# Optimization experiments

Hardware: AMD Instinct MI355X
Metric: run time of the kernel (lower is better)

Reference implementation:

```python
import jax, jax.numpy as jnp
import numpy as np

N_UNARY = 16
N_BINARY = 4
N_NODES = 100000
N_EDGES = 1600000
N_CLAUSES = 8

# Parsed unary clauses: clause i = nU{i}, U{i+1}, U{i+2}
U_IDX = np.array([[i, i + 1, i + 2] for i in range(N_CLAUSES)], dtype=np.int32)
U_SGN = np.tile(np.array([[-1.0, 1.0, 1.0]], dtype=np.float32), (N_CLAUSES, 1))
# Parsed binary clauses over joined matrix [Ux(0:16), Uy(16:32), B(32:36)]:
# clause i = nU{i}x, B{i%4}, U{i}y
B_IDX = np.array([[i, 32 + (i % 4), 16 + i] for i in range(N_CLAUSES)], dtype=np.int32)
B_SGN = np.tile(np.array([[-1.0, 1.0, 1.0]], dtype=np.float32), (N_CLAUSES, 1))


def knowledge_enhancer(x, idx, sgn, w):
    """KENN clause deltas: gather literal columns, softmax(signs*x), scatter-add.
    x: [n, width], idx/sgn: [n_clauses, 3], w: [n_clauses] -> delta [n, width]."""
    sel = x[:, idx] * sgn  # [n, n_clauses, 3]
    d = (w[:, None] * sgn) * jax.nn.softmax(sel, axis=-1)  # [n, n_clauses, 3]
    return jnp.zeros_like(x).at[:, idx].add(d)


def setup_inputs() -> dict:
    key = jax.random.key(0)
    k1, k2, k3, k4 = jax.random.split(key, 4)
    unary = jax.random.normal(k1, (N_NODES, N_UNARY), dtype=jnp.float32)
    binary = jax.random.normal(k2, (N_EDGES, N_BINARY), dtype=jnp.float32)
    index1 = jax.random.randint(k3, (N_EDGES,), 0, N_NODES)
    index2 = jax.random.randint(k4, (N_EDGES,), 0, N_NODES)
    unary_cw = jnp.full((N_CLAUSES,), 0.5, dtype=jnp.float32)
    binary_cw = jnp.full((N_CLAUSES,), 0.5, dtype=jnp.float32)
    return {"unary": unary, "binary": binary, "unary_cw": unary_cw,
            "binary_cw": binary_cw, "index1": index1, "index2": index2}


def reference(unary, binary, unary_cw, binary_cw, index1, index2):
    # Unary knowledge enhancement
    u = unary + knowledge_enhancer(unary, U_IDX, U_SGN, unary_cw)
    # Join: gather endpoint unary features, concat with binary preactivations
    joined = jnp.concatenate([u[index1], u[index2], binary], axis=1)  # [E, 36]
    db = knowledge_enhancer(joined, B_IDX, B_SGN, binary_cw)  # [E, 36]
    # GroupBy: scatter unary parts back to nodes, keep binary part on edges
    delta_up = (jnp.zeros_like(u)
                .at[index1].add(db[:, :N_UNARY])
                .at[index2].add(db[:, N_UNARY:2 * N_UNARY]))
    delta_bp = db[:, 2 * N_UNARY:]
    # activation is identity (default lambda x: x)
    return u + delta_up, binary + delta_bp
```

## Files before the change

### kernel.cpp

```cpp
#include <hip/hip_runtime.h>
#include <math.h>


#define NU 16
#define NC 8
#define TILE_N 400u
#define NB 512
#define BT 512
#define CACHE_N 3200
#define ACC_ST 400
#define BTA 1024

typedef float    f32x4 __attribute__((ext_vector_type(4)));
typedef unsigned u32x4 __attribute__((ext_vector_type(4)));

__device__ __forceinline__ int q10(float x) {
    int q = __float2int_rn(x * 512.0f);
    q = q < -511 ? -511 : (q > 511 ? 511 : q);
    return q & 0x3FF;
}
__device__ __forceinline__ int sx10(unsigned w, int sh) {
    return ((int)(w << (22 - sh))) >> 22;
}
__device__ __forceinline__ unsigned long long pk4(int a0, int a1, int a2, int a3) {
    return (unsigned long long)(long long)a0 +
           ((unsigned long long)(long long)a1 << 16) +
           ((unsigned long long)(long long)a2 << 32) +
           ((unsigned long long)(unsigned short)a3 << 48);
}

__global__ void unary_enhance_kernel(const float* __restrict__ unary,
                                     const float* __restrict__ ucw,
                                     float* __restrict__ out_u,
                                     float* __restrict__ u_lo,
                                     unsigned* __restrict__ cursor,
                                     int n_nodes, int T) {
    int n = blockIdx.x * blockDim.x + threadIdx.x;
    if (cursor && n < T) cursor[n] = 0u;
    if (n >= n_nodes) return;

    float x[NU];
    const float4* src = (const float4*)(unary + (size_t)n * NU);
#pragma unroll
    for (int j = 0; j < 4; ++j) {
        float4 v = src[j];
        x[4*j+0] = v.x; x[4*j+1] = v.y; x[4*j+2] = v.z; x[4*j+3] = v.w;
    }
    float dlt[NU];
#pragma unroll
    for (int j = 0; j < NU; ++j) dlt[j] = 0.0f;
#pragma unroll
    for (int i = 0; i < NC; ++i) {
        float w = ucw[i];
        float a = -x[i], b = x[i+1], c = x[i+2];
        float m = fmaxf(a, fmaxf(b, c));
        float e0 = __expf(a - m);
        float e1 = __expf(b - m);
        float e2 = __expf(c - m);
        float inv = 1.0f / (e0 + e1 + e2);
        dlt[i]   -= w * e0 * inv;
        dlt[i+1] += w * e1 * inv;
        dlt[i+2] += w * e2 * inv;
    }
    float u[NU];
#pragma unroll
    for (int j = 0; j < NU; ++j) u[j] = x[j] + dlt[j];

    float4* dst = (float4*)(out_u + (size_t)n * NU);
#pragma unroll
    for (int j = 0; j < 4; ++j) {
        float4 v; v.x = u[4*j+0]; v.y = u[4*j+1]; v.z = u[4*j+2]; v.w = u[4*j+3];
        dst[j] = v;
    }
    float4* lo = (float4*)(u_lo + (size_t)n * 8);
    float4 l0; l0.x = u[0]; l0.y = u[1]; l0.z = u[2]; l0.w = u[3];
    float4 l1; l1.x = u[4]; l1.y = u[5]; l1.z = u[6]; l1.w = u[7];
    lo[0] = l0; lo[1] = l1;
}

__device__ __forceinline__ void edge_body(int e, int i1, int i2, f32x4 bv,
                                          float4 a0, float4 a1, float4 c0, float4 c1,
                                          const float* w,
                                          float* __restrict__ out_b,
                                          unsigned* hist,
                                          unsigned* __restrict__ entries,
                                          float* __restrict__ out_u,
                                          int cap) {
    float b[4] = {bv.x, bv.y, bv.z, bv.w};
    float u1[8] = {a0.x,a0.y,a0.z,a0.w,a1.x,a1.y,a1.z,a1.w};
    float u2[8] = {c0.x,c0.y,c0.z,c0.w,c1.x,c1.y,c1.z,c1.w};

    float d1[8], d2[8], dbp[4] = {0.f,0.f,0.f,0.f};
#pragma unroll
    for (int i = 0; i < NC; ++i) {
        float a = -u1[i], bb = b[i & 3], c = u2[i];
        float m = fmaxf(a, fmaxf(bb, c));
        float e0x = __expf(a - m);
        float e1x = __expf(bb - m);
        float e2x = __expf(c - m);
        float inv = 1.0f / (e0x + e1x + e2x);
        d1[i] = -w[i] * e0x * inv;
        d2[i] =  w[i] * e2x * inv;
        dbp[i & 3] += w[i] * e1x * inv;
    }
    f32x4 ob;
    ob.x = b[0] + dbp[0];
    ob.y = b[1] + dbp[1];
    ob.z = b[2] + dbp[2];
    ob.w = b[3] + dbp[3];
    __builtin_nontemporal_store(ob, ((f32x4*)out_b) + e);

    unsigned t1 = (unsigned)i1 / TILE_N;
    unsigned id1 = (unsigned)i1 - t1 * TILE_N;
    unsigned slot1 = atomicAdd(&hist[t1], 1u);
    if (slot1 < (unsigned)cap) {
        unsigned* ep = entries + ((size_t)t1 * cap + slot1) * 3;
        ep[0] = (unsigned)q10(d1[0]) | ((unsigned)q10(d1[1]) << 10) | ((unsigned)q10(d1[2]) << 20);
        ep[1] = (unsigned)q10(d1[3]) | ((unsigned)q10(d1[4]) << 10) | ((unsigned)q10(d1[5]) << 20);
        ep[2] = (unsigned)q10(d1[6]) | ((unsigned)q10(d1[7]) << 10) | (id1 << 20);
    } else {
        float* r = out_u + (size_t)i1 * NU;
#pragma unroll
        for (int i = 0; i < NC; ++i) atomicAdd(r + i, d1[i]);
    }

    unsigned t2 = (unsigned)i2 / TILE_N;
    unsigned id2 = (unsigned)i2 - t2 * TILE_N;
    unsigned slot2 = atomicAdd(&hist[t2], 1u);
    if (slot2 < (unsigned)cap) {
        unsigned* ep = entries + ((size_t)t2 * cap + slot2) * 3;
        ep[0] = (unsigned)q10(d2[0]) | ((unsigned)q10(d2[1]) << 10) | ((unsigned)q10(d2[2]) << 20);
        ep[1] = (unsigned)q10(d2[3]) | ((unsigned)q10(d2[4]) << 10) | ((unsigned)q10(d2[5]) << 20);
        ep[2] = (unsigned)q10(d2[6]) | ((unsigned)q10(d2[7]) << 10) | (id2 << 20);
    } else {
        float* r = out_u + (size_t)i2 * NU;
#pragma unroll
        for (int i = 0; i < NC; ++i) atomicAdd(r + i, d2[i]);
    }
}

__global__ __launch_bounds__(BT, 4)
void bin_edges_kernel(const float* __restrict__ binary,
                      const float* __restrict__ bcw,
                      const int* __restrict__ index1,
                      const int* __restrict__ index2,
                      const float* __restrict__ u_lo,
                      float* __restrict__ out_b,
                      unsigned* __restrict__ cursor,
                      unsigned* __restrict__ entries,
                      float* __restrict__ out_u,
                      int n_edges, int T, int cap, int chunk) {
    __shared__ unsigned hist[256];
    __shared__ int ic1[CACHE_N];
    __shared__ int ic2[CACHE_N];
    int tid = threadIdx.x;
    for (int t = tid; t < T; t += BT) hist[t] = 0u;
    __syncthreads();

    int e0 = blockIdx.x * chunk;
    int e1 = e0 + chunk; if (e1 > n_edges) e1 = n_edges;

    for (int e = e0 + tid; e < e1; e += BT) {
        int i1 = __builtin_nontemporal_load(index1 + e);
        int i2 = __builtin_nontemporal_load(index2 + e);
        int l = e - e0;
        ic1[l] = i1;
        ic2[l] = i2;
        atomicAdd(&hist[(unsigned)i1 / TILE_N], 1u);
        atomicAdd(&hist[(unsigned)i2 / TILE_N], 1u);
    }
    __syncthreads();

    for (int t = tid; t < T; t += BT) {
        unsigned c = hist[t];
        unsigned base = 0u;
        if (c) base = atomicAdd(&cursor[t], c);
        hist[t] = base;
    }
    __syncthreads();

    float w[NC];
#pragma unroll
    for (int i = 0; i < NC; ++i) w[i] = bcw[i];

    int eA = e0 + tid;
    for (; eA + 3 * BT < e1; eA += 4 * BT) {
        int eB = eA + BT, eC = eA + 2 * BT, eD = eA + 3 * BT;
        int lA = eA - e0, lB = eB - e0, lC = eC - e0, lD = eD - e0;
        int i1A = ic1[lA], i2A = ic2[lA];
        int i1B = ic1[lB], i2B = ic2[lB];
        int i1C = ic1[lC], i2C = ic2[lC];
        int i1D = ic1[lD], i2D = ic2[lD];

        f32x4 bvA = __builtin_nontemporal_load(((const f32x4*)binary) + eA);
        f32x4 bvB = __builtin_nontemporal_load(((const f32x4*)binary) + eB);
        f32x4 bvC = __builtin_nontemporal_load(((const f32x4*)binary) + eC);
        f32x4 bvD = __builtin_nontemporal_load(((const f32x4*)binary) + eD);

        const float4* p1A = (const float4*)(u_lo + (size_t)i1A * 8);
        const float4* p2A = (const float4*)(u_lo + (size_t)i2A * 8);
        const float4* p1B = (const float4*)(u_lo + (size_t)i1B * 8);
        const float4* p2B = (const float4*)(u_lo + (size_t)i2B * 8);
        const float4* p1C = (const float4*)(u_lo + (size_t)i1C * 8);
        const float4* p2C = (const float4*)(u_lo + (size_t)i2C * 8);
        const float4* p1D = (const float4*)(u_lo + (size_t)i1D * 8);
        const float4* p2D = (const float4*)(u_lo + (size_t)i2D * 8);
        float4 a0A = p1A[0], a1A = p1A[1], c0A = p2A[0], c1A = p2A[1];
        float4 a0B = p1B[0], a1B = p1B[1], c0B = p2B[0], c1B = p2B[1];
        float4 a0C = p1C[0], a1C = p1C[1], c0C = p2C[0], c1C = p2C[1];
        float4 a0D = p1D[0], a1D = p1D[1], c0D = p2D[0], c1D = p2D[1];

        edge_body(eA, i1A, i2A, bvA, a0A, a1A, c0A, c1A,
                  w, out_b, hist, entries, out_u, cap);
        edge_body(eB, i1B, i2B, bvB, a0B, a1B, c0B, c1B,
                  w, out_b, hist, entries, out_u, cap);
        edge_body(eC, i1C, i2C, bvC, a0C, a1C, c0C, c1C,
                  w, out_b, hist, entries, out_u, cap);
        edge_body(eD, i1D, i2D, bvD, a0D, a1D, c0D, c1D,
                  w, out_b, hist, entries, out_u, cap);
    }
    for (; eA < e1; eA += BT) {
        int lA = eA - e0;
        int i1A = ic1[lA], i2A = ic2[lA];
        f32x4 bvA = __builtin_nontemporal_load(((const f32x4*)binary) + eA);
        const float4* p1A = (const float4*)(u_lo + (size_t)i1A * 8);
        const float4* p2A = (const float4*)(u_lo + (size_t)i2A * 8);
        float4 a0A = p1A[0], a1A = p1A[1];
        float4 c0A = p2A[0], c1A = p2A[1];
        edge_body(eA, i1A, i2A, bvA, a0A, a1A, c0A, c1A,
                  w, out_b, hist, entries, out_u, cap);
    }
}

__global__ __launch_bounds__(BTA)
void tile_acc_kernel(const unsigned* __restrict__ cursor,
                     const unsigned* __restrict__ entries,
                     float* __restrict__ out_u,
                     int n_nodes, int cap) {
    __shared__ unsigned long long acc[2 * ACC_ST];
    int t = blockIdx.x;
    int tid = threadIdx.x;
    for (int i = tid; i < 2 * ACC_ST; i += BTA) acc[i] = 0ull;
    __syncthreads();

    unsigned cnt = cursor[t];
    if (cnt > (unsigned)cap) cnt = (unsigned)cap;
    size_t base = (size_t)t * cap;

    unsigned cnt4 = cnt & ~3u;
    for (unsigned i = (unsigned)tid * 4; i < cnt4; i += BTA * 4) {
        const u32x4* p = (const u32x4*)(entries + (base + i) * 3);
        u32x4 q0 = __builtin_nontemporal_load(p + 0);
        u32x4 q1 = __builtin_nontemporal_load(p + 1);
        u32x4 q2 = __builtin_nontemporal_load(p + 2);
        unsigned d[12] = {q0.x, q0.y, q0.z, q0.w,
                          q1.x, q1.y, q1.z, q1.w,
                          q2.x, q2.y, q2.z, q2.w};
#pragma unroll
        for (int k = 0; k < 4; ++k) {
            unsigned wx = d[3*k], wy = d[3*k+1], wz = d[3*k+2];
            unsigned id = wz >> 20;
            unsigned long long lo = pk4(sx10(wx, 0), sx10(wx, 10), sx10(wx, 20), sx10(wy, 0));
            unsigned long long hi = pk4(sx10(wy, 10), sx10(wy, 20), sx10(wz, 0), sx10(wz, 10));
            atomicAdd(&acc[id], lo);
            atomicAdd(&acc[ACC_ST + id], hi);
        }
    }
    for (unsigned i = cnt4 + tid; i < cnt; i += BTA) {
        const unsigned* ep = entries + (base + i) * 3;
        unsigned wx = ep[0], wy = ep[1], wz = ep[2];
        unsigned id = wz >> 20;
        unsigned long long lo = pk4(sx10(wx, 0), sx10(wx, 10), sx10(wx, 20), sx10(wy, 0));
        unsigned long long hi = pk4(sx10(wy, 10), sx10(wy, 20), sx10(wz, 0), sx10(wz, 10));
        atomicAdd(&acc[id], lo);
        atomicAdd(&acc[ACC_ST + id], hi);
    }
    __syncthreads();

    const float INV = 1.0f / 512.0f;
    int nbase = t * (int)TILE_N;
    for (int l = tid; l < (int)TILE_N; l += BTA) {
        int n = nbase + l;
        if (n >= n_nodes) continue;
        float col[8];
#pragma unroll
        for (int wd = 0; wd < 2; ++wd) {
            unsigned long long S = acc[wd*ACC_ST + l];
#pragma unroll
            for (int f = 0; f < 4; ++f) {
                short s = (short)(S & 0xFFFFull);
                col[wd*4 + f] = (float)s * INV;
                S = (S - (unsigned long long)(long long)s) >> 16;
            }
        }
        float4* row = (float4*)(out_u + (size_t)n * NU);
        float4 r0 = row[0], r1 = row[1];
        r0.x += col[0]; r0.y += col[1]; r0.z += col[2]; r0.w += col[3];
        r1.x += col[4]; r1.y += col[5]; r1.z += col[6]; r1.w += col[7];
        row[0] = r0; row[1] = r1;
    }
}

__global__ void edge_enhance_kernel(const float* __restrict__ binary,
                                    const float* __restrict__ bcw,
                                    const int* __restrict__ index1,
                                    const int* __restrict__ index2,
                                    const float* __restrict__ u_lo,
                                    float* __restrict__ out_u,
                                    float* __restrict__ out_b,
                                    int n_edges) {
    int e = blockIdx.x * blockDim.x + threadIdx.x;
    if (e >= n_edges) return;

    int i1 = index1[e];
    int i2 = index2[e];
    float4 bv = ((const float4*)binary)[e];
    float b[4] = {bv.x, bv.y, bv.z, bv.w};

    const float4* p1 = (const float4*)(u_lo + (size_t)i1 * 8);
    float4 a0 = p1[0], a1 = p1[1];
    const float4* p2 = (const float4*)(u_lo + (size_t)i2 * 8);
    float4 c0 = p2[0], c1 = p2[1];
    float u1[8] = {a0.x,a0.y,a0.z,a0.w,a1.x,a1.y,a1.z,a1.w};
    float u2[8] = {c0.x,c0.y,c0.z,c0.w,c1.x,c1.y,c1.z,c1.w};

    float d1[8], d2[8], dbp[4] = {0.f,0.f,0.f,0.f};
#pragma unroll
    for (int i = 0; i < NC; ++i) {
        float w = bcw[i];
        float a = -u1[i], bb = b[i & 3], c = u2[i];
        float m = fmaxf(a, fmaxf(bb, c));
        float e0 = __expf(a - m);
        float e1 = __expf(bb - m);
        float e2 = __expf(c - m);
        float inv = 1.0f / (e0 + e1 + e2);
        d1[i] = -w * e0 * inv;
        d2[i] =  w * e2 * inv;
        dbp[i & 3] += w * e1 * inv;
    }
    float* r1 = out_u + (size_t)i1 * NU;
#pragma unroll
    for (int i = 0; i < NC; ++i) atomicAdd(r1 + i, d1[i]);
    float* r2 = out_u + (size_t)i2 * NU;
#pragma unroll
    for (int i = 0; i < NC; ++i) atomicAdd(r2 + i, d2[i]);

    float4 ob;
    ob.x = b[0] + dbp[0];
    ob.y = b[1] + dbp[1];
    ob.z = b[2] + dbp[2];
    ob.w = b[3] + dbp[3];
    ((float4*)out_b)[e] = ob;
}

extern "C" void kernel_launch(void* const* d_in, const int* in_sizes, int n_in,
                              void* d_out, int out_size, void* d_ws, size_t ws_size,
                              hipStream_t stream) {
    const float* unary  = (const float*)d_in[0];
    const float* binary = (const float*)d_in[1];
    const float* ucw    = (const float*)d_in[2];
    const float* bcw    = (const float*)d_in[3];
    const int*   index1 = (const int*)d_in[4];
    const int*   index2 = (const int*)d_in[5];

    int n_nodes = in_sizes[0] / NU;
    int n_edges = in_sizes[4];

    float* out_u = (float*)d_out;
    float* out_b = out_u + (size_t)n_nodes * NU;

    int T = (int)(((unsigned)n_nodes + TILE_N - 1) / TILE_N);
    size_t mean = (2ull * (size_t)n_edges) / (size_t)T;
    int cap = (int)(mean + mean / 8 + 512);
    cap = (cap + 3) & ~3;

    int chunk = (n_edges + NB - 1) / NB;

    size_t u_lo_bytes  = (size_t)n_nodes * 8 * sizeof(float);
    size_t ent_off     = (u_lo_bytes + 63) & ~(size_t)63;
    size_t ent_bytes   = (size_t)T * cap * 12;
    size_t cur_off     = ent_off + ent_bytes;
    size_t cur_bytes   = (size_t)T * 4;
    size_t need        = cur_off + cur_bytes;

    float* u_lo = (float*)d_ws;
    unsigned* entries = (unsigned*)((char*)d_ws + ent_off);
    unsigned* cursor = (unsigned*)((char*)d_ws + cur_off);

    bool fast = (ws_size >= need && T <= 256 && chunk <= CACHE_N);

    int tb = 256;
    unary_enhance_kernel<<<(n_nodes + tb - 1) / tb, tb, 0, stream>>>(
        unary, ucw, out_u, u_lo, fast ? cursor : (unsigned*)nullptr, n_nodes, T);

    if (fast) {
        bin_edges_kernel<<<NB, BT, 0, stream>>>(
            binary, bcw, index1, index2, u_lo, out_b,
            cursor, entries, out_u, n_edges, T, cap, chunk);
        tile_acc_kernel<<<T, BTA, 0, stream>>>(
            cursor, entries, out_u, n_nodes, cap);
    } else {
        edge_enhance_kernel<<<(n_edges + tb - 1) / tb, tb, 0, stream>>>(
            binary, bcw, index1, index2, u_lo, out_u, out_b, n_edges);
    }
}
```

Before: 183.0 us.

## Replace global cursor binning with fixed per-block slot regions and counts

Drops the histogram pre-pass, the shared-memory index cache and the global atomic cursor reservation. Each edge block now writes its quantized entries straight into a fixed per-(tile, block) region of CAP slots and records per-tile counts at the end. The accumulate kernel scans every slot and skips those beyond each block's count. This removes one pass over the indices plus the global atomics and frees a lot of LDS, but the accumulate pass now reads many unused slots and more overflow edges may fall back to global float atomics.

```diff
diff --git a/kernel.cpp b/kernel.cpp
--- a/kernel.cpp
+++ b/kernel.cpp
@@ -7,9 +7,9 @@
 #define TILE_N 400u
 #define NB 512
 #define BT 512
-#define CACHE_N 3200
 #define ACC_ST 400
 #define BTA 1024
+#define CAP 38
 
 typedef float    f32x4 __attribute__((ext_vector_type(4)));
 typedef unsigned u32x4 __attribute__((ext_vector_type(4)));
@@ -33,10 +33,8 @@
                                      const float* __restrict__ ucw,
                                      float* __restrict__ out_u,
                                      float* __restrict__ u_lo,
-                                     unsigned* __restrict__ cursor,
-                                     int n_nodes, int T) {
+                                     int n_nodes) {
     int n = blockIdx.x * blockDim.x + threadIdx.x;
-    if (cursor && n < T) cursor[n] = 0u;
     if (n >= n_nodes) return;
 
     float x[NU];
@@ -83,9 +81,8 @@
                                           const float* w,
                                           float* __restrict__ out_b,
                                           unsigned* hist,
-                                          unsigned* __restrict__ entries,
-                                          float* __restrict__ out_u,
-                                          int cap) {
+                                          unsigned* __restrict__ eblk,
+                                          float* __restrict__ out_u) {
     float b[4] = {bv.x, bv.y, bv.z, bv.w};
     float u1[8] = {a0.x,a0.y,a0.z,a0.w,a1.x,a1.y,a1.z,a1.w};
     float u2[8] = {c0.x,c0.y,c0.z,c0.w,c1.x,c1.y,c1.z,c1.w};
@@ -113,8 +110,8 @@
     unsigned t1 = (unsigned)i1 / TILE_N;
     unsigned id1 = (unsigned)i1 - t1 * TILE_N;
     unsigned slot1 = atomicAdd(&hist[t1], 1u);
-    if (slot1 < (unsigned)cap) {
-        unsigned* ep = entries + ((size_t)t1 * cap + slot1) * 3;
+    if (slot1 < (unsigned)CAP) {
+        unsigned* ep = eblk + ((size_t)t1 * (NB * CAP) + slot1) * 3;
         ep[0] = (unsigned)q10(d1[0]) | ((unsigned)q10(d1[1]) << 10) | ((unsigned)q10(d1[2]) << 20);
         ep[1] = (unsigned)q10(d1[3]) | ((unsigned)q10(d1[4]) << 10) | ((unsigned)q10(d1[5]) << 20);
         ep[2] = (unsigned)q10(d1[6]) | ((unsigned)q10(d1[7]) << 10) | (id1 << 20);
@@ -127,8 +124,8 @@
     unsigned t2 = (unsigned)i2 / TILE_N;
     unsigned id2 = (unsigned)i2 - t2 * TILE_N;
     unsigned slot2 = atomicAdd(&hist[t2], 1u);
-    if (slot2 < (unsigned)cap) {
-        unsigned* ep = entries + ((size_t)t2 * cap + slot2) * 3;
+    if (slot2 < (unsigned)CAP) {
+        unsigned* ep = eblk + ((size_t)t2 * (NB * CAP) + slot2) * 3;
         ep[0] = (unsigned)q10(d2[0]) | ((unsigned)q10(d2[1]) << 10) | ((unsigned)q10(d2[2]) << 20);
         ep[1] = (unsigned)q10(d2[3]) | ((unsigned)q10(d2[4]) << 10) | ((unsigned)q10(d2[5]) << 20);
         ep[2] = (unsigned)q10(d2[6]) | ((unsigned)q10(d2[7]) << 10) | (id2 << 20);
@@ -146,13 +143,11 @@
                       const int* __restrict__ index2,
                       const float* __restrict__ u_lo,
                       float* __restrict__ out_b,
-                      unsigned* __restrict__ cursor,
+                      unsigned* __restrict__ counts,
                       unsigned* __restrict__ entries,
                       float* __restrict__ out_u,
-                      int n_edges, int T, int cap, int chunk) {
+                      int n_edges, int T, int chunk) {
     __shared__ unsigned hist[256];
-    __shared__ int ic1[CACHE_N];
-    __shared__ int ic2[CACHE_N];
     int tid = threadIdx.x;
     for (int t = tid; t < T; t += BT) hist[t] = 0u;
     __syncthreads();
@@ -160,24 +155,7 @@
     int e0 = blockIdx.x * chunk;
     int e1 = e0 + chunk; if (e1 > n_edges) e1 = n_edges;
 
-    for (int e = e0 + tid; e < e1; e += BT) {
-        int i1 = __builtin_nontemporal_load(index1 + e);
-        int i2 = __builtin_nontemporal_load(index2 + e);
-        int l = e - e0;
-        ic1[l] = i1;
-        ic2[l] = i2;
-        atomicAdd(&hist[(unsigned)i1 / TILE_N], 1u);
-        atomicAdd(&hist[(unsigned)i2 / TILE_N], 1u);
-    }
-    __syncthreads();
-
-    for (int t = tid; t < T; t += BT) {
-        unsigned c = hist[t];
-        unsigned base = 0u;
-        if (c) base = atomicAdd(&cursor[t], c);
-        hist[t] = base;
-    }
-    __syncthreads();
+    unsigned* eblk = entries + (size_t)blockIdx.x * CAP * 3;
 
     float w[NC];
 #pragma unroll
@@ -186,11 +164,14 @@
     int eA = e0 + tid;
     for (; eA + 3 * BT < e1; eA += 4 * BT) {
         int eB = eA + BT, eC = eA + 2 * BT, eD = eA + 3 * BT;
-        int lA = eA - e0, lB = eB - e0, lC = eC - e0, lD = eD - e0;
-        int i1A = ic1[lA], i2A = ic2[lA];
-        int i1B = ic1[lB], i2B = ic2[lB];
-        int i1C = ic1[lC], i2C = ic2[lC];
-        int i1D = ic1[lD], i2D = ic2[lD];
+        int i1A = __builtin_nontemporal_load(index1 + eA);
+        int i2A = __builtin_nontemporal_load(index2 + eA);
+        int i1B = __builtin_nontemporal_load(index1 + eB);
+        int i2B = __builtin_nontemporal_load(index2 + eB);
+        int i1C = __builtin_nontemporal_load(index1 + eC);
+        int i2C = __builtin_nontemporal_load(index2 + eC);
+        int i1D = __builtin_nontemporal_load(index1 + eD);
+        int i2D = __builtin_nontemporal_load(index2 + eD);
 
         f32x4 bvA = __builtin_nontemporal_load(((const f32x4*)binary) + eA);
         f32x4 bvB = __builtin_nontemporal_load(((const f32x4*)binary) + eB);
@@ -210,46 +191,47 @@
         float4 a0C = p1C[0], a1C = p1C[1], c0C = p2C[0], c1C = p2C[1];
         float4 a0D = p1D[0], a1D = p1D[1], c0D = p2D[0], c1D = p2D[1];
 
-        edge_body(eA, i1A, i2A, bvA, a0A, a1A, c0A, c1A,
-                  w, out_b, hist, entries, out_u, cap);
-        edge_body(eB, i1B, i2B, bvB, a0B, a1B, c0B, c1B,
-                  w, out_b, hist, entries, out_u, cap);
-        edge_body(eC, i1C, i2C, bvC, a0C, a1C, c0C, c1C,
-                  w, out_b, hist, entries, out_u, cap);
-        edge_body(eD, i1D, i2D, bvD, a0D, a1D, c0D, c1D,
-                  w, out_b, hist, entries, out_u, cap);
+        edge_body(eA, i1A, i2A, bvA, a0A, a1A, c0A, c1A, w, out_b, hist, eblk, out_u);
+        edge_body(eB, i1B, i2B, bvB, a0B, a1B, c0B, c1B, w, out_b, hist, eblk, out_u);
+        edge_body(eC, i1C, i2C, bvC, a0C, a1C, c0C, c1C, w, out_b, hist, eblk, out_u);
+        edge_body(eD, i1D, i2D, bvD, a0D, a1D, c0D, c1D, w, out_b, hist, eblk, out_u);
     }
     for (; eA < e1; eA += BT) {
-        int lA = eA - e0;
-        int i1A = ic1[lA], i2A = ic2[lA];
+        int i1A = __builtin_nontemporal_load(index1 + eA);
+        int i2A = __builtin_nontemporal_load(index2 + eA);
         f32x4 bvA = __builtin_nontemporal_load(((const f32x4*)binary) + eA);
         const float4* p1A = (const float4*)(u_lo + (size_t)i1A * 8);
         const float4* p2A = (const float4*)(u_lo + (size_t)i2A * 8);
         float4 a0A = p1A[0], a1A = p1A[1];
         float4 c0A = p2A[0], c1A = p2A[1];
-        edge_body(eA, i1A, i2A, bvA, a0A, a1A, c0A, c1A,
-                  w, out_b, hist, entries, out_u, cap);
-    }
+        edge_body(eA, i1A, i2A, bvA, a0A, a1A, c0A, c1A, w, out_b, hist, eblk, out_u);
+    }
+    __syncthreads();
+
+    for (int t = tid; t < T; t += BT) counts[(size_t)t * NB + blockIdx.x] = hist[t];
 }
 
 __global__ __launch_bounds__(BTA)
-void tile_acc_kernel(const unsigned* __restrict__ cursor,
+void tile_acc_kernel(const unsigned* __restrict__ counts,
                      const unsigned* __restrict__ entries,
                      float* __restrict__ out_u,
-                     int n_nodes, int cap) {
+                     int n_nodes) {
     __shared__ unsigned long long acc[2 * ACC_ST];
+    __shared__ unsigned cnt[NB];
     int t = blockIdx.x;
     int tid = threadIdx.x;
     for (int i = tid; i < 2 * ACC_ST; i += BTA) acc[i] = 0ull;
+    for (int i = tid; i < NB; i += BTA) {
+        unsigned c = counts[(size_t)t * NB + i];
+        cnt[i] = c > (unsigned)CAP ? (unsigned)CAP : c;
+    }
     __syncthreads();
 
-    unsigned cnt = cursor[t];
-    if (cnt > (unsigned)cap) cnt = (unsigned)cap;
-    size_t base = (size_t)t * cap;
-
-    unsigned cnt4 = cnt & ~3u;
-    for (unsigned i = (unsigned)tid * 4; i < cnt4; i += BTA * 4) {
-        const u32x4* p = (const u32x4*)(entries + (base + i) * 3);
+    const unsigned total = NB * CAP;
+    const unsigned* base = entries + (size_t)t * NB * CAP * 3;
+
+    for (unsigned j4 = (unsigned)tid * 4; j4 < total; j4 += BTA * 4) {
+        const u32x4* p = (const u32x4*)(base + (size_t)j4 * 3);
         u32x4 q0 = __builtin_nontemporal_load(p + 0);
         u32x4 q1 = __builtin_nontemporal_load(p + 1);
         u32x4 q2 = __builtin_nontemporal_load(p + 2);
@@ -258,6 +240,10 @@
                           q2.x, q2.y, q2.z, q2.w};
 #pragma unroll
         for (int k = 0; k < 4; ++k) {
+            unsigned j = j4 + (unsigned)k;
+            unsigned blk = j / (unsigned)CAP;
+            unsigned slot = j - blk * (unsigned)CAP;
+            if (slot >= cnt[blk]) continue;
             unsigned wx = d[3*k], wy = d[3*k+1], wz = d[3*k+2];
             unsigned id = wz >> 20;
             unsigned long long lo = pk4(sx10(wx, 0), sx10(wx, 10), sx10(wx, 20), sx10(wy, 0));
@@ -265,15 +251,6 @@
             atomicAdd(&acc[id], lo);
             atomicAdd(&acc[ACC_ST + id], hi);
         }
-    }
-    for (unsigned i = cnt4 + tid; i < cnt; i += BTA) {
-        const unsigned* ep = entries + (base + i) * 3;
-        unsigned wx = ep[0], wy = ep[1], wz = ep[2];
-        unsigned id = wz >> 20;
-        unsigned long long lo = pk4(sx10(wx, 0), sx10(wx, 10), sx10(wx, 20), sx10(wy, 0));
-        unsigned long long hi = pk4(sx10(wy, 10), sx10(wy, 20), sx10(wz, 0), sx10(wz, 10));
-        atomicAdd(&acc[id], lo);
-        atomicAdd(&acc[ACC_ST + id], hi);
     }
     __syncthreads();
 
@@ -370,35 +347,31 @@
     float* out_b = out_u + (size_t)n_nodes * NU;
 
     int T = (int)(((unsigned)n_nodes + TILE_N - 1) / TILE_N);
-    size_t mean = (2ull * (size_t)n_edges) / (size_t)T;
-    int cap = (int)(mean + mean / 8 + 512);
-    cap = (cap + 3) & ~3;
-
     int chunk = (n_edges + NB - 1) / NB;
 
     size_t u_lo_bytes  = (size_t)n_nodes * 8 * sizeof(float);
     size_t ent_off     = (u_lo_bytes + 63) & ~(size_t)63;
-    size_t ent_bytes   = (size_t)T * cap * 12;
-    size_t cur_off     = ent_off + ent_bytes;
-    size_t cur_bytes   = (size_t)T * 4;
-    size_t need        = cur_off + cur_bytes;
+    size_t ent_bytes   = (size_t)T * NB * CAP * 12;
+    size_t cnt_off     = ent_off + ent_bytes;
+    size_t cnt_bytes   = (size_t)T * NB * 4;
+    size_t need        = cnt_off + cnt_bytes;
 
     float* u_lo = (float*)d_ws;
     unsigned* entries = (unsigned*)((char*)d_ws + ent_off);
-    unsigned* cursor = (unsigned*)((char*)d_ws + cur_off);
-
-    bool fast = (ws_size >= need && T <= 256 && chunk <= CACHE_N);
+    unsigned* counts  = (unsigned*)((char*)d_ws + cnt_off);
+
+    bool fast = (ws_size >= need && T <= 256 && 2 * chunk <= 25 * T + T / 8);
 
     int tb = 256;
     unary_enhance_kernel<<<(n_nodes + tb - 1) / tb, tb, 0, stream>>>(
-        unary, ucw, out_u, u_lo, fast ? cursor : (unsigned*)nullptr, n_nodes, T);
+        unary, ucw, out_u, u_lo, n_nodes);
 
     if (fast) {
         bin_edges_kernel<<<NB, BT, 0, stream>>>(
             binary, bcw, index1, index2, u_lo, out_b,
-            cursor, entries, out_u, n_edges, T, cap, chunk);
+            counts, entries, out_u, n_edges, T, chunk);
         tile_acc_kernel<<<T, BTA, 0, stream>>>(
-            cursor, entries, out_u, n_nodes, cap);
+            counts, entries, out_u, n_nodes);
     } else {
         edge_enhance_kernel<<<(n_edges + tb - 1) / tb, tb, 0, stream>>>(
             binary, bcw, index1, index2, u_lo, out_u, out_b, n_edges);
```

Result: no change. 184.4 us (+0.8%).
